# Optimization experiments

Measured on AMD Instinct MI355X. Metric: run time of the kernel, lower is better.

Reference implementation:

```python
import jax, jax.numpy as jnp
import numpy as np

NEG_INF = -1e30  # finite stand-in for log(0); keeps grads NaN-free

T_, B_, V_, L_ = 1024, 64, 512, 256


def setup_inputs() -> dict:
    key = jax.random.key(0)
    k1, k2 = jax.random.split(key)
    acts = jax.random.normal(k1, (T_, B_, V_), dtype=jnp.float32)
    labels = jax.random.randint(k2, (B_ * L_,), 1, V_, dtype=jnp.int32)  # blank=0 excluded
    act_lens = jnp.full((B_,), T_, dtype=jnp.int32)
    label_lens = jnp.full((B_,), L_, dtype=jnp.int32)
    return {"acts": acts, "labels": labels, "act_lens": act_lens, "label_lens": label_lens}


def _ctc_total_loss(acts, labels, act_lens, label_lens):
    # acts: (T, B, V) raw logits; warp-ctc applies softmax internally.
    T, B, V = acts.shape
    L = labels.shape[0] // B          # static max label length (uniform lengths)
    S = 2 * L + 1                     # extended label lattice with interleaved blanks
    logp = jax.nn.log_softmax(acts, axis=-1)

    # Unflatten labels -> padded (B, L)
    offsets = jnp.concatenate([jnp.zeros((1,), jnp.int32),
                               jnp.cumsum(label_lens.astype(jnp.int32))])[:-1]
    j = jnp.arange(L, dtype=jnp.int32)
    gidx = jnp.clip(offsets[:, None] + j[None, :], 0, labels.shape[0] - 1)
    padded = jnp.where(j[None, :] < label_lens[:, None], labels[gidx], 0)  # (B, L)

    # Extended labels: blank, l1, blank, l2, ..., blank
    ext = jnp.zeros((B, S), dtype=labels.dtype).at[:, 1::2].set(padded)
    ext_m2 = jnp.pad(ext, ((0, 0), (2, 0)))[:, :S]
    allow_skip = (ext != 0) & (ext != ext_m2)
    allow_skip = allow_skip.at[:, :2].set(False)

    bidx = jnp.arange(B)[:, None]
    lp_ext = logp[:, bidx, ext]       # (T, B, S): per-frame log-prob of lattice states

    alpha0 = jnp.full((B, S), NEG_INF, dtype=acts.dtype)
    alpha0 = alpha0.at[:, 0].set(lp_ext[0, :, 0]).at[:, 1].set(lp_ext[0, :, 1])
    neg = jnp.full((B, 1), NEG_INF, dtype=acts.dtype)

    def step(alpha, inp):
        lp_t, t = inp
        a1 = alpha
        a2 = jnp.concatenate([neg, alpha[:, :-1]], axis=1)
        a3 = jnp.concatenate([neg, neg, alpha[:, :-2]], axis=1)
        a3 = jnp.where(allow_skip, a3, NEG_INF)
        new = lp_t + jnp.logaddexp(jnp.logaddexp(a1, a2), a3)
        alpha = jnp.where((t < act_lens)[:, None], new, alpha)  # freeze past act_len
        return alpha, None

    alpha, _ = jax.lax.scan(step, alpha0, (lp_ext[1:], jnp.arange(1, T)))

    s_end = (2 * label_lens).astype(jnp.int32)           # final blank state
    a_end = jnp.take_along_axis(alpha, s_end[:, None], axis=1)[:, 0]
    a_end2 = jnp.take_along_axis(alpha, jnp.maximum(s_end - 1, 0)[:, None], axis=1)[:, 0]
    losses = -jnp.logaddexp(a_end, a_end2)               # per-example NLL
    return jnp.sum(losses)[None]                         # shape (1,), matches FloatTensor([sum])


def reference(acts, labels, act_lens, label_lens):
    return _ctc_total_loss(acts, labels, act_lens, label_lens)
```

## Files before the change

kernel.cpp:

```cpp
#include <hip/hip_runtime.h>

constexpr int T = 1024;
constexpr int B = 64;
constexpr int V = 512;
constexpr int L = 256;
constexpr int S = 2 * L + 1;
constexpr int C = 16;

typedef float f32x4 __attribute__((ext_vector_type(4)));

__device__ __forceinline__ unsigned short f2bf(float f) {
    unsigned u = __float_as_uint(f);
    u += 0x7fffu + ((u >> 16) & 1u);
    return (unsigned short)(u >> 16);
}

__device__ __forceinline__ float lane_bcast(float v, int i) {
    return __uint_as_float((unsigned)__builtin_amdgcn_readlane((int)__float_as_uint(v), i));
}

__device__ __forceinline__ float dpp_shr1z(float x) {
    return __uint_as_float((unsigned)__builtin_amdgcn_update_dpp(
        0, (int)__float_as_uint(x), 0x138, 0xf, 0xf, true));
}
__device__ __forceinline__ float dpp_shl1z(float x) {
    return __uint_as_float((unsigned)__builtin_amdgcn_update_dpp(
        0, (int)__float_as_uint(x), 0x130, 0xf, 0xf, true));
}
template <int CTRL, int RM>
__device__ __forceinline__ float dppmax(float m) {
    int mi = (int)__float_as_uint(m);
    int t = __builtin_amdgcn_update_dpp(mi, mi, CTRL, RM, 0xf, false);
    return fmaxf(m, __uint_as_float((unsigned)t));
}
template <int CTRL, int RM>
__device__ __forceinline__ float dppadd(float m) {
    int mi = (int)__float_as_uint(m);
    int t = __builtin_amdgcn_update_dpp(0, mi, CTRL, RM, 0xf, true);
    return m + __uint_as_float((unsigned)t);
}
#define DPPMAX_LADDER(m) do {                                                 \
        m = dppmax<0x111, 0xf>(m); m = dppmax<0x112, 0xf>(m);                 \
        m = dppmax<0x114, 0xf>(m); m = dppmax<0x118, 0xf>(m);                 \
        m = dppmax<0x142, 0xa>(m); m = dppmax<0x143, 0xc>(m);                 \
    } while (0)
#define DPPADD_LADDER(m) do {                                                 \
        m = dppadd<0x111, 0xf>(m); m = dppadd<0x112, 0xf>(m);                 \
        m = dppadd<0x114, 0xf>(m); m = dppadd<0x118, 0xf>(m);                 \
        m = dppadd<0x142, 0xa>(m); m = dppadd<0x143, 0xc>(m);                 \
    } while (0)


__global__ __launch_bounds__(64) void offsets_kernel(
    const int* __restrict__ label_lens, int* __restrict__ offsets)
{
    int lane = threadIdx.x;
    int v = (lane < B) ? label_lens[lane] : 0;
    int x = v;
#pragma unroll
    for (int o = 1; o < 64; o <<= 1) {
        int y = __shfl_up(x, o, 64);
        if (lane >= o) x += y;
    }
    if (lane < B) offsets[lane] = x - v;
}

__global__ __launch_bounds__(256) void setup_kernel(
    const float* __restrict__ acts, const int* __restrict__ labels,
    const int* __restrict__ label_lens, const int* __restrict__ offsets,
    float* __restrict__ lse_rows, unsigned short* __restrict__ packedU,
    float* __restrict__ blankU)
{
    __shared__ float rows[4][2][V];
    const int w    = threadIdx.x >> 6;
    const int lane = threadIdx.x & 63;
    const int rbase = (blockIdx.x * 4 + w) * 2;
    const f32x4* p = (const f32x4*)(acts + (size_t)rbase * V);

    f32x4 xa0 = __builtin_nontemporal_load(p + lane);
    f32x4 xa1 = __builtin_nontemporal_load(p + lane + 64);
    f32x4 xb0 = __builtin_nontemporal_load(p + lane + 128);
    f32x4 xb1 = __builtin_nontemporal_load(p + lane + 192);
    f32x4 ea0, ea1, eb0, eb1;
    ea0.x=__expf(xa0.x); ea0.y=__expf(xa0.y); ea0.z=__expf(xa0.z); ea0.w=__expf(xa0.w);
    ea1.x=__expf(xa1.x); ea1.y=__expf(xa1.y); ea1.z=__expf(xa1.z); ea1.w=__expf(xa1.w);
    eb0.x=__expf(xb0.x); eb0.y=__expf(xb0.y); eb0.z=__expf(xb0.z); eb0.w=__expf(xb0.w);
    eb1.x=__expf(xb1.x); eb1.y=__expf(xb1.y); eb1.z=__expf(xb1.z); eb1.w=__expf(xb1.w);
    ((f32x4*)rows[w][0])[lane]      = ea0;
    ((f32x4*)rows[w][0])[lane + 64] = ea1;
    ((f32x4*)rows[w][1])[lane]      = eb0;
    ((f32x4*)rows[w][1])[lane + 64] = eb1;
    float sa = ea0.x+ea0.y+ea0.z+ea0.w + ea1.x+ea1.y+ea1.z+ea1.w;
    float sb = eb0.x+eb0.y+eb0.z+eb0.w + eb1.x+eb1.y+eb1.z+eb1.w;
#pragma unroll
    for (int o = 32; o; o >>= 1) { sa += __shfl_xor(sa, o, 64); sb += __shfl_xor(sb, o, 64); }

#pragma unroll
    for (int rr = 0; rr < 2; ++rr) {
        const int r = rbase + rr;
        const int b = r & (B - 1), t = r >> 6;
        const float* rw = rows[w][rr];
        const int lab_len = label_lens[b];
        const int off     = offsets[b];
        const float ubk   = rw[0];
        const int j0 = 4 * lane;
        float q0 = (j0 + 0 < lab_len) ? rw[labels[min(off + j0 + 0, B * L - 1)]] : ubk;
        float q1 = (j0 + 1 < lab_len) ? rw[labels[min(off + j0 + 1, B * L - 1)]] : ubk;
        float q2 = (j0 + 2 < lab_len) ? rw[labels[min(off + j0 + 2, B * L - 1)]] : ubk;
        float q3 = (j0 + 3 < lab_len) ? rw[labels[min(off + j0 + 3, B * L - 1)]] : ubk;
        ushort4 hv = {f2bf(q0), f2bf(q1), f2bf(q2), f2bf(q3)};
        ((ushort4*)packedU)[(size_t)(b * T + t) * 64 + lane] = hv;
        if (lane == 0) {
            lse_rows[b * T + t] = __logf(rr ? sb : sa);
            blankU[b * T + t]   = ubk;
        }
    }
}

__global__ __launch_bounds__(128, 1) void ctc_kernel(
    const int* __restrict__ labels, const int* __restrict__ act_lens,
    const int* __restrict__ label_lens, const int* __restrict__ offsets,
    const float* __restrict__ lse_rows, const unsigned short* __restrict__ packedU,
    const float* __restrict__ blankU, float* __restrict__ out)
{
    __shared__ float sbr[S];
    __shared__ float s_accb;

    const int b    = blockIdx.x;
    const int wave = threadIdx.x >> 6;
    const int lane = threadIdx.x & 63;
    const int lab_len = label_lens[b];
    const int a_len   = act_lens[b];
    const int th      = (a_len - 1) >> 1;
    const int thp1    = th + 1;
    const int off     = offsets[b];
    const size_t rowbase = (size_t)b * T;

    int li0 = 4 * lane;
    int eprev = (li0 - 1 >= 0 && li0 - 1 < lab_len) ? labels[min(off + li0 - 1, B * L - 1)] : 0;
    int enext = (li0 + 4 < lab_len) ? labels[min(off + li0 + 4, B * L - 1)] : 0;
    int e0 = (li0 + 0 < lab_len) ? labels[min(off + li0 + 0, B * L - 1)] : 0;
    int e1 = (li0 + 1 < lab_len) ? labels[min(off + li0 + 1, B * L - 1)] : 0;
    int e2 = (li0 + 2 < lab_len) ? labels[min(off + li0 + 2, B * L - 1)] : 0;
    int e3 = (li0 + 3 < lab_len) ? labels[min(off + li0 + 3, B * L - 1)] : 0;

    const float aF0 = (8 * lane + 1 >= 2 && e0 != 0 && e0 != eprev) ? 1.f : 0.f;
    const float aF1 = (e1 != 0 && e1 != e0) ? 1.f : 0.f;
    const float aF2 = (e2 != 0 && e2 != e1) ? 1.f : 0.f;
    const float aF3 = (e3 != 0 && e3 != e2) ? 1.f : 0.f;
    const float aB0 = aF1, aB1 = aF2, aB2 = aF3;
    const float aB3 = (enext != 0 && enext != e3) ? 1.f : 0.f;

    float A0 = 0.f, A1 = 0.f, A2 = 0.f, A3 = 0.f, A4 = 0.f,
          A5 = 0.f, A6 = 0.f, A7 = 0.f, A8 = 0.f;
    float acc = 0.f, sls = 0.f;

    uint2 a_0,a_1,a_2,a_3,a_4,a_5,a_6,a_7,a_8,a_9,a_10,a_11,a_12,a_13,a_14,a_15;
    uint2 b_0,b_1,b_2,b_3,b_4,b_5,b_6,b_7,b_8,b_9,b_10,b_11,b_12,b_13,b_14,b_15;
    uint2 c_0,c_1,c_2,c_3,c_4,c_5,c_6,c_7,c_8,c_9,c_10,c_11,c_12,c_13,c_14,c_15;
    float a_K = 0.f, b_K = 0.f, c_K = 0.f;

#define PINV(x) asm volatile("" : "+v"(x))
#define APPLY16(M, P) M(P,0) M(P,1) M(P,2) M(P,3) M(P,4) M(P,5) M(P,6) M(P,7) \
                      M(P,8) M(P,9) M(P,10) M(P,11) M(P,12) M(P,13) M(P,14) M(P,15)

#define LD1(P, I) P##_##I = gp_[(I) * 64 + lane];
#define LOADCH(P, TLO) do {                                                   \
        const int tl_ = min(max((int)(TLO), 0), T - C);                       \
        const uint2* gp_ = (const uint2*)(packedU + (rowbase + tl_) * 256);   \
        APPLY16(LD1, P)                                                       \
        P##_K = blankU[rowbase + tl_ + (lane & (C - 1))];                     \
    } while (0)

#define PIN1(P, I) PINV(P##_##I.x); PINV(P##_##I.y);
#define PINCH(P) do { APPLY16(PIN1, P) PINV(P##_K); } while (0)

#define RESCALE() do {                                                        \
        float m_ = fmaxf(A8, A0); m_ = fmaxf(m_, A1); m_ = fmaxf(m_, A2);     \
        m_ = fmaxf(m_, A3); m_ = fmaxf(m_, A4); m_ = fmaxf(m_, A5);           \
        m_ = fmaxf(m_, A6); m_ = fmaxf(m_, A7);                               \
        DPPMAX_LADDER(m_);                                                    \
        m_ = lane_bcast(m_, 63);                                              \
        m_ = fmaxf(m_, 1e-30f);                                               \
        float inv_ = __builtin_amdgcn_rcpf(m_);                               \
        acc += __logf(m_);                                                    \
        A0 *= inv_; A1 *= inv_; A2 *= inv_; A3 *= inv_; A4 *= inv_;           \
        A5 *= inv_; A6 *= inv_; A7 *= inv_; A8 *= inv_;                       \
    } while (0)

#define STEPF_CORE(HX, HY, UB) do {                                           \
        const float ub_ = (UB);                                               \
        const unsigned hx_ = (HX), hy_ = (HY);                                \
        const float u0_ = __uint_as_float(hx_ << 16);                         \
        const float u1_ = __uint_as_float(hx_ & 0xffff0000u);                 \
        const float u2_ = __uint_as_float(hy_ << 16);                         \
        const float u3_ = __uint_as_float(hy_ & 0xffff0000u);                 \
        const float pA7_ = dpp_shr1z(A7);                                     \
        A8 = ub_ * (A8 + A7);                                                 \
        A7 = u3_ * fmaf(aF3, A5, A7 + A6);                                    \
        A6 = ub_ * (A6 + A5);                                                 \
        A5 = u2_ * fmaf(aF2, A3, A5 + A4);                                    \
        A4 = ub_ * (A4 + A3);                                                 \
        A3 = u1_ * fmaf(aF1, A1, A3 + A2);                                    \
        A2 = ub_ * (A2 + A1);                                                 \
        A1 = u0_ * fmaf(aF0, pA7_, A1 + A0);                                  \
        A0 = ub_ * (A0 + pA7_);                                               \
    } while (0)

#define STEPB_CORE(HX, HY, UB) do {                                           \
        const float ub_ = (UB);                                               \
        const unsigned hx_ = (HX), hy_ = (HY);                                \
        const float u0_ = __uint_as_float(hx_ << 16);                         \
        const float u1_ = __uint_as_float(hx_ & 0xffff0000u);                 \
        const float u2_ = __uint_as_float(hy_ << 16);                         \
        const float u3_ = __uint_as_float(hy_ & 0xffff0000u);                 \
        const float nC0_ = dpp_shl1z(A0);                                     \
        A8 = ub_ * (A8 + A0);                                                 \
        A0 = u0_ * fmaf(aB0, A2, A0 + A1);                                    \
        A1 = ub_ * (A1 + A2);                                                 \
        A2 = u1_ * fmaf(aB1, A4, A2 + A3);                                    \
        A3 = ub_ * (A3 + A4);                                                 \
        A4 = u2_ * fmaf(aB2, A6, A4 + A5);                                    \
        A5 = ub_ * (A5 + A6);                                                 \
        A6 = u3_ * fmaf(aB3, nC0_, A6 + A7);                                  \
        A7 = ub_ * (A7 + nC0_);                                               \
    } while (0)

#define SF(P, I)  STEPF_CORE(P##_##I.x, P##_##I.y, lane_bcast(P##_K, I));
#define SB(P, I)  STEPB_CORE(P##_##I.x, P##_##I.y, lane_bcast(P##_K, I));
#define SFG(P, I, TLO) if ((TLO) + (I) <= th)   { SF(P, I) }
#define SBG(P, I, TLO) if ((TLO) + (I) >= thp1) { SB(P, I) }

#define DOF16(P) do {                                                         \
        SF(P,0) SF(P,1) SF(P,2) SF(P,3) SF(P,4) SF(P,5) SF(P,6) SF(P,7)       \
        RESCALE();                                                            \
        SF(P,8) SF(P,9) SF(P,10) SF(P,11) SF(P,12) SF(P,13) SF(P,14) SF(P,15) \
        RESCALE();                                                            \
    } while (0)
#define DOFPART(P, TLO) do {                                                  \
        SFG(P,0,TLO) SFG(P,1,TLO) SFG(P,2,TLO) SFG(P,3,TLO)                   \
        SFG(P,4,TLO) SFG(P,5,TLO) SFG(P,6,TLO) SFG(P,7,TLO)                   \
        RESCALE();                                                            \
        SFG(P,8,TLO) SFG(P,9,TLO) SFG(P,10,TLO) SFG(P,11,TLO)                 \
        SFG(P,12,TLO) SFG(P,13,TLO) SFG(P,14,TLO) SFG(P,15,TLO)               \
        RESCALE();                                                            \
    } while (0)
#define DOB16(P) do {                                                         \
        SB(P,15) SB(P,14) SB(P,13) SB(P,12) SB(P,11) SB(P,10) SB(P,9) SB(P,8) \
        RESCALE();                                                            \
        SB(P,7) SB(P,6) SB(P,5) SB(P,4) SB(P,3) SB(P,2) SB(P,1) SB(P,0)       \
        RESCALE();                                                            \
    } while (0)
#define DOBPART(P, TLO) do {                                                  \
        SBG(P,15,TLO) SBG(P,14,TLO) SBG(P,13,TLO) SBG(P,12,TLO)               \
        SBG(P,11,TLO) SBG(P,10,TLO) SBG(P,9,TLO) SBG(P,8,TLO)                 \
        RESCALE();                                                            \
        SBG(P,7,TLO) SBG(P,6,TLO) SBG(P,5,TLO) SBG(P,4,TLO)                   \
        SBG(P,3,TLO) SBG(P,2,TLO) SBG(P,1,TLO) SBG(P,0,TLO)                   \
        RESCALE();                                                            \
    } while (0)

#define STEP_DIRECT(WHICH, TT) do {                                           \
        uint2 hvd_ = ((const uint2*)(packedU + (rowbase + (TT)) * 256))[lane];\
        float ubd_ = blankU[rowbase + (TT)];                                  \
        WHICH(hvd_.x, hvd_.y, ubd_);                                          \
    } while (0)

    if (wave == 0) {
        if (lane == 0) {
            A0 = blankU[rowbase];
            A1 = __uint_as_float(((unsigned)packedU[rowbase * 256]) << 16);
        }

        if (th >= 1) {
            const int nst   = th;
            const int nc    = (nst + C - 1) / C;
            const int nfull = nst / C;
            LOADCH(a, 1);
            LOADCH(b, 1 + C);
            LOADCH(c, 1 + 2 * C);

            if (a_len == T) {
                const f32x4* lp = (const f32x4*)(lse_rows + rowbase);
                f32x4 s0 = lp[lane], s1 = lp[lane + 64],
                      s2 = lp[lane + 128], s3 = lp[lane + 192];
                float s = s0.x+s0.y+s0.z+s0.w + s1.x+s1.y+s1.z+s1.w
                        + s2.x+s2.y+s2.z+s2.w + s3.x+s3.y+s3.z+s3.w;
                DPPADD_LADDER(s);
                sls = lane_bcast(s, 63);
            } else {
                for (int t = lane; t < a_len; t += 64) sls += lse_rows[rowbase + t];
#pragma unroll
                for (int o = 32; o; o >>= 1) sls += __shfl_xor(sls, o, 64);
            }

            int cc = 0;
            for (; cc + 3 <= nfull; cc += 3) {
                PINCH(a); DOF16(a); LOADCH(a, 1 + C * (cc + 3));
                PINCH(b); DOF16(b); LOADCH(b, 1 + C * (cc + 4));
                PINCH(c); DOF16(c); LOADCH(c, 1 + C * (cc + 5));
            }
            const int rem = nfull - cc;
            if (rem == 0) {
                if (nc > nfull) { PINCH(a); DOFPART(a, 1 + C * cc); }
            } else if (rem == 1) {
                PINCH(a); DOF16(a);
                if (nc > nfull) { PINCH(b); DOFPART(b, 1 + C * (cc + 1)); }
            } else {
                PINCH(a); DOF16(a);
                PINCH(b); DOF16(b);
                if (nc > nfull) { PINCH(c); DOFPART(c, 1 + C * (cc + 2)); }
            }
        } else {
            for (int t = lane; t < a_len; t += 64) sls += lse_rows[rowbase + t];
#pragma unroll
            for (int o = 32; o; o >>= 1) sls += __shfl_xor(sls, o, 64);
        }
    } else {
        const int send = 2 * lab_len;
        {
            size_t rl = rowbase + (a_len - 1);
            float ubl = blankU[rl];
            float ue  = (lab_len > 0)
                      ? __uint_as_float(((unsigned)packedU[rl * 256 + (lab_len - 1)]) << 16)
                      : 0.f;
            int s0 = 8 * lane + 1;
            A0 = (s0 + 0 == send) ? ubl : ((s0 + 0 == send - 1) ? ue : 0.f);
            A1 = (s0 + 1 == send) ? ubl : ((s0 + 1 == send - 1) ? ue : 0.f);
            A2 = (s0 + 2 == send) ? ubl : ((s0 + 2 == send - 1) ? ue : 0.f);
            A3 = (s0 + 3 == send) ? ubl : ((s0 + 3 == send - 1) ? ue : 0.f);
            A4 = (s0 + 4 == send) ? ubl : ((s0 + 4 == send - 1) ? ue : 0.f);
            A5 = (s0 + 5 == send) ? ubl : ((s0 + 5 == send - 1) ? ue : 0.f);
            A6 = (s0 + 6 == send) ? ubl : ((s0 + 6 == send - 1) ? ue : 0.f);
            A7 = (s0 + 7 == send) ? ubl : ((s0 + 7 == send - 1) ? ue : 0.f);
            A8 = (send == 0) ? ubl : 0.f;
        }

        const int nstB = a_len - 2 - th;
        if (nstB > 0 && a_len >= 17) {
            const int nc    = (nstB + C - 1) / C;
            const int nfull = nstB / C;
            LOADCH(a, a_len - 17);
            LOADCH(b, a_len - 17 - C);
            LOADCH(c, a_len - 17 - 2 * C);
            int cc = 0;
            for (; cc + 3 <= nfull; cc += 3) {
                PINCH(a); DOB16(a); LOADCH(a, a_len - 17 - C * (cc + 3));
                PINCH(b); DOB16(b); LOADCH(b, a_len - 17 - C * (cc + 4));
                PINCH(c); DOB16(c); LOADCH(c, a_len - 17 - C * (cc + 5));
            }
            const int rem = nfull - cc;
            if (rem == 0) {
                if (nc > nfull) { PINCH(a); DOBPART(a, a_len - 17 - C * cc); }
            } else if (rem == 1) {
                PINCH(a); DOB16(a);
                if (nc > nfull) { PINCH(b); DOBPART(b, a_len - 17 - C * (cc + 1)); }
            } else {
                PINCH(a); DOB16(a);
                PINCH(b); DOB16(b);
                if (nc > nfull) { PINCH(c); DOBPART(c, a_len - 17 - C * (cc + 2)); }
            }
        } else if (nstB > 0) {
            for (int t = a_len - 2; t >= thp1; --t) {
                STEP_DIRECT(STEPB_CORE, t);
                if (((a_len - 2 - t) & 7) == 7) RESCALE();
            }
        }

        {
            float nC0 = dpp_shl1z(A0);
            float w1 = fmaf(aB0, A2, A0 + A1);
            float w2 = A1 + A2;
            float w3 = fmaf(aB1, A4, A2 + A3);
            float w4 = A3 + A4;
            float w5 = fmaf(aB2, A6, A4 + A5);
            float w6 = A5 + A6;
            float w7 = fmaf(aB3, nC0, A6 + A7);
            float w8 = A7 + nC0;
            int sB = 8 * lane + 1;
            sbr[sB + 0] = w1; sbr[sB + 1] = w2; sbr[sB + 2] = w3; sbr[sB + 3] = w4;
            sbr[sB + 4] = w5; sbr[sB + 5] = w6; sbr[sB + 6] = w7; sbr[sB + 7] = w8;
            if (lane == 0) sbr[0] = A8 + A0;
            if (lane == 0) s_accb = acc;
        }
    }
    __syncthreads();
    if (wave == 0) {
        int s0 = 8 * lane;
        float p0 = __logf(fmaxf(A0, 1e-37f)) + __logf(fmaxf(sbr[s0 + 0], 1e-37f));
        float p1 = __logf(fmaxf(A1, 1e-37f)) + __logf(fmaxf(sbr[s0 + 1], 1e-37f));
        float p2 = __logf(fmaxf(A2, 1e-37f)) + __logf(fmaxf(sbr[s0 + 2], 1e-37f));
        float p3 = __logf(fmaxf(A3, 1e-37f)) + __logf(fmaxf(sbr[s0 + 3], 1e-37f));
        float p4 = __logf(fmaxf(A4, 1e-37f)) + __logf(fmaxf(sbr[s0 + 4], 1e-37f));
        float p5 = __logf(fmaxf(A5, 1e-37f)) + __logf(fmaxf(sbr[s0 + 5], 1e-37f));
        float p6 = __logf(fmaxf(A6, 1e-37f)) + __logf(fmaxf(sbr[s0 + 6], 1e-37f));
        float p7 = __logf(fmaxf(A7, 1e-37f)) + __logf(fmaxf(sbr[s0 + 7], 1e-37f));
        float p8 = -3.0e38f;
        if (lane == 63) p8 = __logf(fmaxf(A8, 1e-37f)) + __logf(fmaxf(sbr[512], 1e-37f));
        float pmax = fmaxf(fmaxf(fmaxf(p0, p1), fmaxf(p2, p3)),
                           fmaxf(fmaxf(p4, p5), fmaxf(p6, p7)));
        pmax = fmaxf(pmax, p8);
        DPPMAX_LADDER(pmax);
        pmax = lane_bcast(pmax, 63);
        float dot = __expf(p0 - pmax) + __expf(p1 - pmax) + __expf(p2 - pmax)
                  + __expf(p3 - pmax) + __expf(p4 - pmax) + __expf(p5 - pmax)
                  + __expf(p6 - pmax) + __expf(p7 - pmax);
        if (lane == 63) dot += __expf(p8 - pmax);
        DPPADD_LADDER(dot);
        dot = lane_bcast(dot, 63);
        if (lane == 0) {
            float loss = sls - acc - s_accb - (pmax + __logf(dot));
            atomicAdd(out, loss);
        }
    }
#undef PINV
#undef APPLY16
#undef LD1
#undef LOADCH
#undef PIN1
#undef PINCH
#undef RESCALE
#undef STEPF_CORE
#undef STEPB_CORE
#undef SF
#undef SB
#undef SFG
#undef SBG
#undef DOF16
#undef DOFPART
#undef DOB16
#undef DOBPART
#undef STEP_DIRECT
}

extern "C" void kernel_launch(void* const* d_in, const int* in_sizes, int n_in,
                              void* d_out, int out_size, void* d_ws, size_t ws_size,
                              hipStream_t stream) {
    const float* acts       = (const float*)d_in[0];
    const int*   labels     = (const int*)d_in[1];
    const int*   act_lens   = (const int*)d_in[2];
    const int*   label_lens = (const int*)d_in[3];
    float*       out        = (float*)d_out;

    float*          lse_rows = (float*)d_ws;
    float*          blankU   = (float*)((char*)d_ws + (size_t)T * B * 4);
    int*            offsets  = (int*)  ((char*)d_ws + (size_t)2 * T * B * 4);
    unsigned short* packedU  = (unsigned short*)((char*)d_ws + (1u << 20));

    hipMemsetAsync(d_out, 0, sizeof(float), stream);

    offsets_kernel<<<1, 64, 0, stream>>>(label_lens, offsets);
    setup_kernel<<<T * B / 8, 256, 0, stream>>>(
        acts, labels, label_lens, offsets, lse_rows, packedU, blankU);
    ctc_kernel<<<B, 128, 0, stream>>>(
        labels, act_lens, label_lens, offsets, lse_rows, packedU, blankU, out);
}
```

Before: 243.8 us.

## Fold blank probability out of recurrence by normalizing label probs per frame

```diff
diff --git a/kernel.cpp b/kernel.cpp
--- a/kernel.cpp
+++ b/kernel.cpp
@@ -68,8 +68,8 @@
 __global__ __launch_bounds__(256) void setup_kernel(
     const float* __restrict__ acts, const int* __restrict__ labels,
     const int* __restrict__ label_lens, const int* __restrict__ offsets,
-    float* __restrict__ lse_rows, unsigned short* __restrict__ packedU,
-    float* __restrict__ blankU)
+    float* __restrict__ lse_rows, unsigned short* __restrict__ packedR,
+    float* __restrict__ blankU, float* __restrict__ logub)
 {
     __shared__ float rows[4][2][V];
     const int w    = threadIdx.x >> 6;
@@ -95,6 +95,9 @@
 #pragma unroll
     for (int o = 32; o; o >>= 1) { sa += __shfl_xor(sa, o, 64); sb += __shfl_xor(sb, o, 64); }
 
+    const float xblk0 = lane_bcast(xa0.x, 0);
+    const float xblk1 = lane_bcast(xb0.x, 0);
+
 #pragma unroll
     for (int rr = 0; rr < 2; ++rr) {
         const int r = rbase + rr;
@@ -103,16 +106,18 @@
         const int lab_len = label_lens[b];
         const int off     = offsets[b];
         const float ubk   = rw[0];
+        const float rub   = __builtin_amdgcn_rcpf(ubk);
         const int j0 = 4 * lane;
-        float q0 = (j0 + 0 < lab_len) ? rw[labels[min(off + j0 + 0, B * L - 1)]] : ubk;
-        float q1 = (j0 + 1 < lab_len) ? rw[labels[min(off + j0 + 1, B * L - 1)]] : ubk;
-        float q2 = (j0 + 2 < lab_len) ? rw[labels[min(off + j0 + 2, B * L - 1)]] : ubk;
-        float q3 = (j0 + 3 < lab_len) ? rw[labels[min(off + j0 + 3, B * L - 1)]] : ubk;
+        float q0 = (j0 + 0 < lab_len) ? rw[labels[min(off + j0 + 0, B * L - 1)]] * rub : 1.f;
+        float q1 = (j0 + 1 < lab_len) ? rw[labels[min(off + j0 + 1, B * L - 1)]] * rub : 1.f;
+        float q2 = (j0 + 2 < lab_len) ? rw[labels[min(off + j0 + 2, B * L - 1)]] * rub : 1.f;
+        float q3 = (j0 + 3 < lab_len) ? rw[labels[min(off + j0 + 3, B * L - 1)]] * rub : 1.f;
         ushort4 hv = {f2bf(q0), f2bf(q1), f2bf(q2), f2bf(q3)};
-        ((ushort4*)packedU)[(size_t)(b * T + t) * 64 + lane] = hv;
+        ((ushort4*)packedR)[(size_t)(b * T + t) * 64 + lane] = hv;
         if (lane == 0) {
             lse_rows[b * T + t] = __logf(rr ? sb : sa);
             blankU[b * T + t]   = ubk;
+            logub[b * T + t]    = rr ? xblk1 : xblk0;
         }
     }
 }
@@ -120,8 +125,9 @@
 __global__ __launch_bounds__(128, 1) void ctc_kernel(
     const int* __restrict__ labels, const int* __restrict__ act_lens,
     const int* __restrict__ label_lens, const int* __restrict__ offsets,
-    const float* __restrict__ lse_rows, const unsigned short* __restrict__ packedU,
-    const float* __restrict__ blankU, float* __restrict__ out)
+    const float* __restrict__ lse_rows, const unsigned short* __restrict__ packedR,
+    const float* __restrict__ blankU, const float* __restrict__ logub,
+    float* __restrict__ out)
 {
     __shared__ float sbr[S];
     __shared__ float s_accb;
@@ -153,12 +159,11 @@
 
     float A0 = 0.f, A1 = 0.f, A2 = 0.f, A3 = 0.f, A4 = 0.f,
           A5 = 0.f, A6 = 0.f, A7 = 0.f, A8 = 0.f;
-    float acc = 0.f, sls = 0.f;
+    float acc = 0.f, sls = 0.f, slog = 0.f;
 
     uint2 a_0,a_1,a_2,a_3,a_4,a_5,a_6,a_7,a_8,a_9,a_10,a_11,a_12,a_13,a_14,a_15;
     uint2 b_0,b_1,b_2,b_3,b_4,b_5,b_6,b_7,b_8,b_9,b_10,b_11,b_12,b_13,b_14,b_15;
     uint2 c_0,c_1,c_2,c_3,c_4,c_5,c_6,c_7,c_8,c_9,c_10,c_11,c_12,c_13,c_14,c_15;
-    float a_K = 0.f, b_K = 0.f, c_K = 0.f;
 
 #define PINV(x) asm volatile("" : "+v"(x))
 #define APPLY16(M, P) M(P,0) M(P,1) M(P,2) M(P,3) M(P,4) M(P,5) M(P,6) M(P,7) \
@@ -167,13 +172,12 @@
 #define LD1(P, I) P##_##I = gp_[(I) * 64 + lane];
 #define LOADCH(P, TLO) do {                                                   \
         const int tl_ = min(max((int)(TLO), 0), T - C);                       \
-        const uint2* gp_ = (const uint2*)(packedU + (rowbase + tl_) * 256);   \
+        const uint2* gp_ = (const uint2*)(packedR + (rowbase + tl_) * 256);   \
         APPLY16(LD1, P)                                                       \
-        P##_K = blankU[rowbase + tl_ + (lane & (C - 1))];                     \
     } while (0)
 
 #define PIN1(P, I) PINV(P##_##I.x); PINV(P##_##I.y);
-#define PINCH(P) do { APPLY16(PIN1, P) PINV(P##_K); } while (0)
+#define PINCH(P) do { APPLY16(PIN1, P) } while (0)
 
 #define RESCALE() do {                                                        \
         float m_ = fmaxf(A8, A0); m_ = fmaxf(m_, A1); m_ = fmaxf(m_, A2);     \
@@ -188,46 +192,44 @@
         A5 *= inv_; A6 *= inv_; A7 *= inv_; A8 *= inv_;                       \
     } while (0)
 
-#define STEPF_CORE(HX, HY, UB) do {                                           \
-        const float ub_ = (UB);                                               \
+#define STEPF_CORE(HX, HY) do {                                               \
         const unsigned hx_ = (HX), hy_ = (HY);                                \
         const float u0_ = __uint_as_float(hx_ << 16);                         \
         const float u1_ = __uint_as_float(hx_ & 0xffff0000u);                 \
         const float u2_ = __uint_as_float(hy_ << 16);                         \
         const float u3_ = __uint_as_float(hy_ & 0xffff0000u);                 \
         const float pA7_ = dpp_shr1z(A7);                                     \
-        A8 = ub_ * (A8 + A7);                                                 \
+        A8 = A8 + A7;                                                         \
         A7 = u3_ * fmaf(aF3, A5, A7 + A6);                                    \
-        A6 = ub_ * (A6 + A5);                                                 \
+        A6 = A6 + A5;                                                         \
         A5 = u2_ * fmaf(aF2, A3, A5 + A4);                                    \
-        A4 = ub_ * (A4 + A3);                                                 \
+        A4 = A4 + A3;                                                         \
         A3 = u1_ * fmaf(aF1, A1, A3 + A2);                                    \
-        A2 = ub_ * (A2 + A1);                                                 \
+        A2 = A2 + A1;                                                         \
         A1 = u0_ * fmaf(aF0, pA7_, A1 + A0);                                  \
-        A0 = ub_ * (A0 + pA7_);                                               \
-    } while (0)
-
-#define STEPB_CORE(HX, HY, UB) do {                                           \
-        const float ub_ = (UB);                                               \
+        A0 = A0 + pA7_;                                                       \
+    } while (0)
+
+#define STEPB_CORE(HX, HY) do {                                               \
         const unsigned hx_ = (HX), hy_ = (HY);                                \
         const float u0_ = __uint_as_float(hx_ << 16);                         \
         const float u1_ = __uint_as_float(hx_ & 0xffff0000u);                 \
         const float u2_ = __uint_as_float(hy_ << 16);                         \
         const float u3_ = __uint_as_float(hy_ & 0xffff0000u);                 \
         const float nC0_ = dpp_shl1z(A0);                                     \
-        A8 = ub_ * (A8 + A0);                                                 \
+        A8 = A8 + A0;                                                         \
         A0 = u0_ * fmaf(aB0, A2, A0 + A1);                                    \
-        A1 = ub_ * (A1 + A2);                                                 \
+        A1 = A1 + A2;                                                         \
         A2 = u1_ * fmaf(aB1, A4, A2 + A3);                                    \
-        A3 = ub_ * (A3 + A4);                                                 \
+        A3 = A3 + A4;                                                         \
         A4 = u2_ * fmaf(aB2, A6, A4 + A5);                                    \
-        A5 = ub_ * (A5 + A6);                                                 \
+        A5 = A5 + A6;                                                         \
         A6 = u3_ * fmaf(aB3, nC0_, A6 + A7);                                  \
-        A7 = ub_ * (A7 + nC0_);                                               \
-    } while (0)
-
-#define SF(P, I)  STEPF_CORE(P##_##I.x, P##_##I.y, lane_bcast(P##_K, I));
-#define SB(P, I)  STEPB_CORE(P##_##I.x, P##_##I.y, lane_bcast(P##_K, I));
+        A7 = A7 + nC0_;                                                       \
+    } while (0)
+
+#define SF(P, I)  STEPF_CORE(P##_##I.x, P##_##I.y);
+#define SB(P, I)  STEPB_CORE(P##_##I.x, P##_##I.y);
 #define SFG(P, I, TLO) if ((TLO) + (I) <= th)   { SF(P, I) }
 #define SBG(P, I, TLO) if ((TLO) + (I) >= thp1) { SB(P, I) }
 
@@ -261,15 +263,14 @@
     } while (0)
 
 #define STEP_DIRECT(WHICH, TT) do {                                           \
-        uint2 hvd_ = ((const uint2*)(packedU + (rowbase + (TT)) * 256))[lane];\
-        float ubd_ = blankU[rowbase + (TT)];                                  \
-        WHICH(hvd_.x, hvd_.y, ubd_);                                          \
+        uint2 hvd_ = ((const uint2*)(packedR + (rowbase + (TT)) * 256))[lane];\
+        WHICH(hvd_.x, hvd_.y);                                                \
     } while (0)
 
     if (wave == 0) {
         if (lane == 0) {
             A0 = blankU[rowbase];
-            A1 = __uint_as_float(((unsigned)packedU[rowbase * 256]) << 16);
+            A1 = __uint_as_float(((unsigned)packedR[rowbase * 256]) << 16) * A0;
         }
 
         if (th >= 1) {
@@ -282,16 +283,30 @@
 
             if (a_len == T) {
                 const f32x4* lp = (const f32x4*)(lse_rows + rowbase);
+                const f32x4* gp = (const f32x4*)(logub + rowbase);
                 f32x4 s0 = lp[lane], s1 = lp[lane + 64],
                       s2 = lp[lane + 128], s3 = lp[lane + 192];
+                f32x4 g0 = gp[lane], g1 = gp[lane + 64],
+                      g2 = gp[lane + 128], g3 = gp[lane + 192];
                 float s = s0.x+s0.y+s0.z+s0.w + s1.x+s1.y+s1.z+s1.w
                         + s2.x+s2.y+s2.z+s2.w + s3.x+s3.y+s3.z+s3.w;
-                DPPADD_LADDER(s);
-                sls = lane_bcast(s, 63);
+                float g = g0.x+g0.y+g0.z+g0.w + g1.x+g1.y+g1.z+g1.w
+                        + g2.x+g2.y+g2.z+g2.w + g3.x+g3.y+g3.z+g3.w;
+                DPPADD_LADDER(s); DPPADD_LADDER(g);
+                sls  = lane_bcast(s, 63);
+                slog = lane_bcast(g, 63) - logub[rowbase] - logub[rowbase + T - 1];
             } else {
-                for (int t = lane; t < a_len; t += 64) sls += lse_rows[rowbase + t];
+                float g = 0.f;
+                for (int t = lane; t < a_len; t += 64) {
+                    sls += lse_rows[rowbase + t];
+                    if (t >= 1 && t <= a_len - 2) g += logub[rowbase + t];
+                }
 #pragma unroll
-                for (int o = 32; o; o >>= 1) sls += __shfl_xor(sls, o, 64);
+                for (int o = 32; o; o >>= 1) {
+                    sls += __shfl_xor(sls, o, 64);
+                    g   += __shfl_xor(g, o, 64);
+                }
+                slog = g;
             }
 
             int cc = 0;
@@ -312,9 +327,17 @@
                 if (nc > nfull) { PINCH(c); DOFPART(c, 1 + C * (cc + 2)); }
             }
         } else {
-            for (int t = lane; t < a_len; t += 64) sls += lse_rows[rowbase + t];
+            float g = 0.f;
+            for (int t = lane; t < a_len; t += 64) {
+                sls += lse_rows[rowbase + t];
+                if (t >= 1 && t <= a_len - 2) g += logub[rowbase + t];
+            }
 #pragma unroll
-            for (int o = 32; o; o >>= 1) sls += __shfl_xor(sls, o, 64);
+            for (int o = 32; o; o >>= 1) {
+                sls += __shfl_xor(sls, o, 64);
+                g   += __shfl_xor(g, o, 64);
+            }
+            slog = g;
         }
     } else {
         const int send = 2 * lab_len;
@@ -322,7 +345,7 @@
             size_t rl = rowbase + (a_len - 1);
             float ubl = blankU[rl];
             float ue  = (lab_len > 0)
-                      ? __uint_as_float(((unsigned)packedU[rl * 256 + (lab_len - 1)]) << 16)
+                      ? __uint_as_float(((unsigned)packedR[rl * 256 + (lab_len - 1)]) << 16) * ubl
                       : 0.f;
             int s0 = 8 * lane + 1;
             A0 = (s0 + 0 == send) ? ubl : ((s0 + 0 == send - 1) ? ue : 0.f);
@@ -409,7 +432,7 @@
         DPPADD_LADDER(dot);
         dot = lane_bcast(dot, 63);
         if (lane == 0) {
-            float loss = sls - acc - s_accb - (pmax + __logf(dot));
+            float loss = sls - slog - acc - s_accb - (pmax + __logf(dot));
             atomicAdd(out, loss);
         }
     }
@@ -445,13 +468,14 @@
     float*          lse_rows = (float*)d_ws;
     float*          blankU   = (float*)((char*)d_ws + (size_t)T * B * 4);
     int*            offsets  = (int*)  ((char*)d_ws + (size_t)2 * T * B * 4);
-    unsigned short* packedU  = (unsigned short*)((char*)d_ws + (1u << 20));
+    float*          logub    = (float*)((char*)d_ws + (size_t)3 * T * B * 4);
+    unsigned short* packedR  = (unsigned short*)((char*)d_ws + (1u << 20));
 
     hipMemsetAsync(d_out, 0, sizeof(float), stream);
 
     offsets_kernel<<<1, 64, 0, stream>>>(label_lens, offsets);
     setup_kernel<<<T * B / 8, 256, 0, stream>>>(
-        acts, labels, label_lens, offsets, lse_rows, packedU, blankU);
+        acts, labels, label_lens, offsets, lse_rows, packedR, blankU, logub);
     ctc_kernel<<<B, 128, 0, stream>>>(
-        labels, act_lens, label_lens, offsets, lse_rows, packedU, blankU, out);
-}
+        labels, act_lens, label_lens, offsets, lse_rows, packedR, blankU, logub, out);
+}
```

Measured after the change: 236.1 us. 1.03x faster.
